# Kernel tuning notes

Hardware: AMD Instinct MI355X
Metric: run time of the kernel (lower is better)

Reference implementation:

```python
import jax, jax.numpy as jnp
import numpy as np

NUM_HEADS = 16
D_MODEL = 1024
D_DEPTH = D_MODEL // NUM_HEADS
B, Q_LEN, M_LEN = 4, 1024, 1024
K_LEN = Q_LEN + M_LEN


def setup_inputs() -> dict:
    key = jax.random.key(0)
    ks = jax.random.split(key, 8)
    return {
        "inputs": jax.random.normal(ks[0], (B, Q_LEN, D_MODEL), jnp.float32),
        "pos_emb": jax.random.normal(ks[1], (1, K_LEN, D_MODEL), jnp.float32),
        "r_w_bias": jax.random.normal(ks[2], (NUM_HEADS, D_DEPTH), jnp.float32) * 0.01,
        "r_r_bias": jax.random.normal(ks[3], (NUM_HEADS, D_DEPTH), jnp.float32) * 0.01,
        "mems": jax.random.normal(ks[4], (B, M_LEN, D_MODEL), jnp.float32),
        "W_w": jax.random.normal(ks[5], (D_MODEL, 3 * D_MODEL), jnp.float32) * 0.01,
        "W_r": jax.random.normal(ks[6], (D_MODEL, D_MODEL), jnp.float32) * 0.01,
        "W_o": jax.random.normal(ks[7], (D_MODEL, D_MODEL), jnp.float32) * 0.01,
    }


def relative_shift(x):
    # x: [b, n, q, k] -> left-shift row i by (q - 1 - i) via pad/reshape/slice trick
    b, n, q, k = x.shape
    x = jnp.pad(x, ((0, 0), (0, 0), (0, 0), (1, 0)))
    x = x.reshape(b, n, k + 1, q)
    x = x[:, :, 1:, :]
    return x.reshape(b, n, q, k)


def relative_mask(q_len, m_len, dtype):
    # [q, m+q]: 1 at/left of current position, 0 to the right
    k = m_len + q_len
    return (jnp.arange(k)[None, :] <= (m_len + jnp.arange(q_len))[:, None]).astype(dtype)


def reference(inputs, pos_emb, r_w_bias, r_r_bias, mems, W_w, W_r, W_o):
    b, q_len, d_model = inputs.shape
    cat = jnp.concatenate([mems, inputs], axis=1)            # [b, k, d]
    k_len = cat.shape[1]
    m_len = k_len - q_len
    pe = pos_emb[:, -k_len:]                                  # [1, k, d]

    w_heads = (cat @ W_w).reshape(b, k_len, 3 * NUM_HEADS, D_DEPTH)
    w_head_q, w_head_k, w_head_v = jnp.split(w_heads, 3, axis=2)  # each [b,k,n,dd]
    w_head_q = w_head_q[:, -q_len:]                           # [b,q,n,dd]

    ac = jnp.einsum('bqnd,bknd->bnqk', w_head_q + r_w_bias, w_head_k)

    r_head_k = (pe[0] @ W_r).reshape(k_len, NUM_HEADS, D_DEPTH)
    bd = jnp.einsum('bqnd,knd->bnqk', w_head_q + r_r_bias, r_head_k)
    bd = relative_shift(bd)

    mask = relative_mask(q_len, m_len, ac.dtype)              # [q, k]
    score = (ac + bd) / jnp.asarray(D_DEPTH ** 0.5, ac.dtype)
    score = score * mask - 1e30 * (1.0 - mask)
    attn = jax.nn.softmax(score, axis=-1)

    attn_vec = jnp.einsum('bnqk,bknd->bqnd', attn, w_head_v)
    attn_vec = attn_vec.reshape(b, q_len, d_model)
    return attn_vec @ W_o
```

## Files before the change

### kernel.cpp

```cpp
#include <hip/hip_runtime.h>
#include <cstdint>
#include <cstddef>

static constexpr int QL = 1024;

typedef _Float16 half8 __attribute__((ext_vector_type(8)));
typedef _Float16 half4 __attribute__((ext_vector_type(4)));
typedef float f32x4 __attribute__((ext_vector_type(4)));

__device__ __forceinline__ const float* gemm_row_ptr(const float* A, const float* A2,
                                                     int r, int gather) {
  if (!gather) return A + (size_t)r * 1024;
  int b = r >> 11, tt = r & 2047;
  if (tt < QL) return A + ((size_t)b * QL + tt) * 1024;
  return A2 + ((size_t)b * QL + (tt - QL)) * 1024;
}

__global__ __launch_bounds__(256) void convert_a16(
    const float* __restrict__ A, const float* __restrict__ A2, int gather,
    _Float16* __restrict__ dst) {
  const int row = blockIdx.x;
  const int c = threadIdx.x * 4;
  const float* src = gemm_row_ptr(A, A2, row, gather);
  float4 v = *(const float4*)(src + c);
  half4 o = { (_Float16)v.x, (_Float16)v.y, (_Float16)v.z, (_Float16)v.w };
  *(half4*)(dst + (size_t)row * 1024 + c) = o;
}

__global__ __launch_bounds__(256) void split_w(
    const float* __restrict__ W, _Float16* __restrict__ Wt, int N) {
  __shared__ float T[64][65];
  const int nb = blockIdx.x * 64, kb = blockIdx.y * 64;
  const int t = threadIdx.x;
  {
    int row = t >> 2, c0 = (t & 3) * 16;
    const float* src = W + (size_t)(kb + row) * N + nb + c0;
#pragma unroll
    for (int c = 0; c < 16; c += 4) {
      float4 v = *(const float4*)(src + c);
      T[row][c0 + c + 0] = v.x; T[row][c0 + c + 1] = v.y;
      T[row][c0 + c + 2] = v.z; T[row][c0 + c + 3] = v.w;
    }
  }
  __syncthreads();
  {
    int nrow = t >> 2, ks = (t & 3) * 16;
    half8 hi0, hi1, lo0, lo1;
#pragma unroll
    for (int c = 0; c < 16; ++c) {
      float f = T[ks + c][nrow];
      _Float16 h = (_Float16)f;
      _Float16 l = (_Float16)(f - (float)h);
      if (c < 8) { hi0[c] = h; lo0[c] = l; } else { hi1[c - 8] = h; lo1[c - 8] = l; }
    }
    int kglob = kb + ks;
    int kt = kglob >> 5, pos = kglob & 31;
    _Float16* dst = Wt + (size_t)(nb + nrow) * 2048 + kt * 64 + pos;
    *(half8*)dst = hi0; *(half8*)(dst + 8) = hi1;
    *(half8*)(dst + 32) = lo0; *(half8*)(dst + 40) = lo1;
  }
}

__global__ __launch_bounds__(256) void gemm2(
    const _Float16* __restrict__ A16, const _Float16* __restrict__ Bt,
    int mode, const float* __restrict__ rwb,
    _Float16* __restrict__ d_q, _Float16* __restrict__ d_k,
    _Float16* __restrict__ d_v, float* __restrict__ d_f) {
  const int nbase = blockIdx.x * 128, mbase = blockIdx.y * 128;
  if (mode == 0 && nbase < 1024 && (mbase & 1024) == 0) return;

  __shared__ __align__(16) _Float16 As[128][40];
  __shared__ __align__(16) _Float16 Bs[128][72];
  const int t = threadIdx.x;
  const int lane = t & 63, w = t >> 6;
  const int ln = lane & 15, g = lane >> 4;
  const int wm = (w & 1) * 64, wn = (w >> 1) * 64;
  const int ar = t >> 1, aseg = (t & 1) * 16;
  const int br = t >> 1;
  const int bseg = (mode == 2) ? (t & 1) * 32 : (t & 1) * 16;
  const _Float16* arow = A16 + (size_t)(mbase + ar) * 1024 + aseg;
  const _Float16* brow = Bt + (size_t)(nbase + br) * 2048 + bseg;

  half8 pa0, pa1, pb0, pb1, pb2, pb3;
  pa0 = *(const half8*)(arow);      pa1 = *(const half8*)(arow + 8);
  pb0 = *(const half8*)(brow);      pb1 = *(const half8*)(brow + 8);
  if (mode == 2) { pb2 = *(const half8*)(brow + 16); pb3 = *(const half8*)(brow + 24); }

  f32x4 acc[4][4] = {};
  for (int kt = 0; kt < 32; ++kt) {
    __syncthreads();
    *(half8*)&As[ar][aseg] = pa0;     *(half8*)&As[ar][aseg + 8] = pa1;
    *(half8*)&Bs[br][bseg] = pb0;     *(half8*)&Bs[br][bseg + 8] = pb1;
    if (mode == 2) { *(half8*)&Bs[br][bseg + 16] = pb2; *(half8*)&Bs[br][bseg + 24] = pb3; }
    __syncthreads();
    if (kt + 1 < 32) {
      const _Float16* ap = arow + (kt + 1) * 32;
      const _Float16* bp = brow + (kt + 1) * 64;
      pa0 = *(const half8*)(ap);      pa1 = *(const half8*)(ap + 8);
      pb0 = *(const half8*)(bp);      pb1 = *(const half8*)(bp + 8);
      if (mode == 2) { pb2 = *(const half8*)(bp + 16); pb3 = *(const half8*)(bp + 24); }
    }
    half8 ah[4], bh[4], bl[4];
#pragma unroll
    for (int i = 0; i < 4; ++i)
      ah[i] = *(const half8*)&As[wm + i * 16 + ln][g * 8];
#pragma unroll
    for (int j = 0; j < 4; ++j)
      bh[j] = *(const half8*)&Bs[wn + j * 16 + ln][g * 8];
    if (mode == 2) {
#pragma unroll
      for (int j = 0; j < 4; ++j)
        bl[j] = *(const half8*)&Bs[wn + j * 16 + ln][32 + g * 8];
    }
#pragma unroll
    for (int i = 0; i < 4; ++i)
#pragma unroll
      for (int j = 0; j < 4; ++j) {
        acc[i][j] = __builtin_amdgcn_mfma_f32_16x16x32_f16(ah[i], bh[j], acc[i][j], 0, 0, 0);
        if (mode == 2)
          acc[i][j] = __builtin_amdgcn_mfma_f32_16x16x32_f16(ah[i], bl[j], acc[i][j], 0, 0, 0);
      }
  }

  if (mode == 2) {
#pragma unroll
    for (int i = 0; i < 4; ++i)
#pragma unroll
      for (int j = 0; j < 4; ++j) {
        float* cp = d_f + (size_t)(mbase + wm + i * 16 + g * 4) * 1024 + nbase + wn + j * 16 + ln;
#pragma unroll
        for (int r = 0; r < 4; ++r) cp[(size_t)r * 1024] = acc[i][j][r];
      }
    return;
  }
  if (mode == 1) {
#pragma unroll
    for (int j = 0; j < 4; ++j) {
      int n = nbase + wn + j * 16 + ln;
      int h = n >> 6, d = n & 63;
#pragma unroll
      for (int i = 0; i < 4; ++i) {
        int m0 = mbase + wm + i * 16 + g * 4;
        _Float16* rp = d_q + ((size_t)h * 2048 + m0) * 64 + d;
#pragma unroll
        for (int r = 0; r < 4; ++r) rp[(size_t)r * 64] = (_Float16)acc[i][j][r];
      }
    }
    return;
  }
#pragma unroll
  for (int j = 0; j < 4; ++j) {
    int n = nbase + wn + j * 16 + ln;
    int sec = n >> 10;
    int c2 = n & 1023, h = c2 >> 6, d = c2 & 63;
    float bias = (sec == 0) ? rwb[c2] : 0.f;
#pragma unroll
    for (int i = 0; i < 4; ++i) {
      int m0 = mbase + wm + i * 16 + g * 4;
      int b = m0 >> 11, tt0 = m0 & 2047;
      size_t bh = (size_t)(b * 16 + h);
#pragma unroll
      for (int r = 0; r < 4; ++r) {
        int tt = tt0 + r;
        float v = acc[i][j][r];
        if (sec == 0) {
          if (tt >= 1024)
            d_q[(bh * 1024 + (tt - 1024)) * 64 + d] = (_Float16)(v + bias);
        } else if (sec == 1) {
          d_k[(bh * 2048 + tt) * 64 + d] = (_Float16)v;
        } else {
          d_v[(bh * 64 + d) * 2048 + tt] = (_Float16)v;
        }
      }
    }
  }
}

__global__ __launch_bounds__(256) void cdelta_kernel(
    const _Float16* __restrict__ r16, const float* __restrict__ rwb,
    const float* __restrict__ rrb, float* __restrict__ cd) {
  int idx = blockIdx.x * 256 + threadIdx.x;
  int jr = idx >> 4, h = idx & 15;
  const _Float16* rp = r16 + ((size_t)h * 2048 + jr) * 64;
  const float* a = rrb + h * 64;
  const float* b = rwb + h * 64;
  float s = 0.f;
#pragma unroll 8
  for (int d = 0; d < 64; ++d) s += (a[d] - b[d]) * (float)rp[d];
  cd[h * 2048 + jr] = s;
}

__global__ __launch_bounds__(256) void attn_mfma3(
    const _Float16* __restrict__ qw16, const _Float16* __restrict__ k16,
    const _Float16* __restrict__ vt16, const _Float16* __restrict__ r16,
    const float* __restrict__ cdelta, _Float16* __restrict__ av16) {
  __shared__ __align__(16) float scratch[4][80][21];
  __shared__ __align__(16) _Float16 k_s[64][72];
  __shared__ __align__(16) _Float16 vt_s[64][72];
  __shared__ __align__(16) _Float16 r_s[128][72];
  __shared__ __align__(16) _Float16 P_s[4][16][72];
  __shared__ float cdw_s[128];
  _Float16 (*qw_s)[72] = (_Float16 (*)[72])&scratch[0][0][0];

  const int id = blockIdx.x;
  const int hb = id & 63, pr = id >> 6;
  const int h = hb >> 2, b = hb & 3;
  const int bh = b * 16 + h;
  const int t = threadIdx.x;
  const int lane = t & 63, w = t >> 6;
  const int ln = lane & 15, g = lane >> 4;
  const int rb = 48 - 16 * w;

  const int s_row4 = t >> 2, s_c16 = (t & 3) * 16;
  const int s_row2 = t >> 1, s_c32 = (t & 1) * 32;

  const float* cdh = cdelta + h * 2048;
  const _Float16* kb_p = k16 + (size_t)bh * 2048 * 64;
  const _Float16* vb_p = vt16 + (size_t)bh * 64 * 2048;
  const _Float16* rb_p = r16 + (size_t)h * 2048 * 64;
  const _Float16* qb_p = qw16 + (size_t)bh * 1024 * 64;

#pragma unroll 1
  for (int phase = 0; phase < 2; ++phase) {
    const int qt = phase ? (15 - pr) : pr;
    const int qbase = qt * 64;
    const int ktiles = qt + 17;
    const int R0 = 960 - qbase;

    __syncthreads();
    {
      const _Float16* src = qb_p + (size_t)(qbase + s_row4) * 64 + s_c16;
      half8 a0 = *(const half8*)src;
      half8 a1 = *(const half8*)(src + 8);
      *(half8*)&qw_s[s_row4][s_c16] = a0;
      *(half8*)&qw_s[s_row4][s_c16 + 8] = a1;
    }
    __syncthreads();
    half8 aq0 = *(const half8*)&qw_s[16 * w + ln][g * 8];
    half8 aq1 = *(const half8*)&qw_s[16 * w + ln][32 + g * 8];
    __syncthreads();

    f32x4 O[4] = {};
    float llane[4] = {0.f, 0.f, 0.f, 0.f};

    half8 kp0, kp1, vp0, vp1, rp0, rp1, rp2, rp3;
    float cdp = 0.f;
    {
      const _Float16* kp = kb_p + (size_t)s_row4 * 64 + s_c16;
      kp0 = *(const half8*)kp; kp1 = *(const half8*)(kp + 8);
      const _Float16* vp = vb_p + (size_t)s_row4 * 2048 + s_c16;
      vp0 = *(const half8*)vp; vp1 = *(const half8*)(vp + 8);
      int rr = R0 + s_row2; rr = rr > 2047 ? 2047 : rr;
      const _Float16* rp = rb_p + (size_t)rr * 64 + s_c32;
      rp0 = *(const half8*)rp;        rp1 = *(const half8*)(rp + 8);
      rp2 = *(const half8*)(rp + 16); rp3 = *(const half8*)(rp + 24);
      if (t < 128) { int cr = R0 + t; cr = cr > 2047 ? 2047 : cr; cdp = cdh[cr]; }
    }

    for (int kt = 0; kt < ktiles; ++kt) {
      const int kbase = kt * 64;
      const int koff = (kt & 1) * 64;
      __syncthreads();
      *(half8*)&k_s[s_row4][s_c16] = kp0;  *(half8*)&k_s[s_row4][s_c16 + 8] = kp1;
      *(half8*)&vt_s[s_row4][s_c16] = vp0; *(half8*)&vt_s[s_row4][s_c16 + 8] = vp1;
      if (kt == 0) {
        *(half8*)&r_s[s_row2][s_c32] = rp0;      *(half8*)&r_s[s_row2][s_c32 + 8] = rp1;
        *(half8*)&r_s[s_row2][s_c32 + 16] = rp2; *(half8*)&r_s[s_row2][s_c32 + 24] = rp3;
        if (t < 128) cdw_s[t] = cdp;
      } else {
        const int sb = 64 - koff;
        *(half8*)&r_s[sb + s_row4][s_c16] = rp0;
        *(half8*)&r_s[sb + s_row4][s_c16 + 8] = rp1;
        if (t < 64) cdw_s[sb + t] = cdp;
      }
      __syncthreads();
      if (kt + 1 < ktiles) {
        const int kb2 = kbase + 64;
        const _Float16* kp = kb_p + (size_t)(kb2 + s_row4) * 64 + s_c16;
        kp0 = *(const half8*)kp; kp1 = *(const half8*)(kp + 8);
        const _Float16* vp = vb_p + (size_t)s_row4 * 2048 + kb2 + s_c16;
        vp0 = *(const half8*)vp; vp1 = *(const half8*)(vp + 8);
        int rr = R0 + kbase + 128 + s_row4; rr = rr > 2047 ? 2047 : rr;
        const _Float16* rp = rb_p + (size_t)rr * 64 + s_c16;
        rp0 = *(const half8*)rp; rp1 = *(const half8*)(rp + 8);
        if (t < 64) { int cr = R0 + kbase + 128 + t; cr = cr > 2047 ? 2047 : cr; cdp = cdh[cr]; }
      }

      f32x4 Sf[4];
#pragma unroll
      for (int jt = 0; jt < 4; ++jt) {
        half8 b0 = *(const half8*)&k_s[jt * 16 + ln][g * 8];
        half8 b1 = *(const half8*)&k_s[jt * 16 + ln][32 + g * 8];
        f32x4 z = {0.f, 0.f, 0.f, 0.f};
        z = __builtin_amdgcn_mfma_f32_16x16x32_f16(aq0, b0, z, 0, 0, 0);
        z = __builtin_amdgcn_mfma_f32_16x16x32_f16(aq1, b1, z, 0, 0, 0);
        Sf[jt] = z;
      }
#pragma unroll
      for (int ft = 0; ft < 5; ++ft) {
        int rrow = (rb + ft * 16 + ln + koff) & 127;
        half8 b0 = *(const half8*)&r_s[rrow][g * 8];
        half8 b1 = *(const half8*)&r_s[rrow][32 + g * 8];
        f32x4 z = {0.f, 0.f, 0.f, 0.f};
        z = __builtin_amdgcn_mfma_f32_16x16x32_f16(aq0, b0, z, 0, 0, 0);
        z = __builtin_amdgcn_mfma_f32_16x16x32_f16(aq1, b1, z, 0, 0, 0);
        float cdv = cdw_s[rrow];
        float* sc = &scratch[w][ft * 16 + ln][0];
        sc[4 * g + 0] = z[0] + cdv; sc[4 * g + 1] = z[1] + cdv;
        sc[4 * g + 2] = z[2] + cdv; sc[4 * g + 3] = z[3] + cdv;
      }
      const int climit = qbase + 16 * w + 1039 - kbase;
#pragma unroll
      for (int r = 0; r < 4; ++r) {
        float psum = 0.f;
#pragma unroll
        for (int jt = 0; jt < 4; ++jt) {
          int cw = jt * 16 + ln + 15 - 4 * g - r;
          float tv = scratch[w][cw][4 * g + r];
          float x = (Sf[jt][r] + tv) * 0.125f;
          float p = (cw > climit) ? 0.f : __expf(x);
          psum += p;
          P_s[w][4 * g + r][jt * 16 + ln] = (_Float16)p;
        }
        llane[r] += psum;
      }
      half8 pA0 = *(const half8*)&P_s[w][ln][g * 8];
      half8 pA1 = *(const half8*)&P_s[w][ln][32 + g * 8];
#pragma unroll
      for (int dt = 0; dt < 4; ++dt) {
        half8 b0 = *(const half8*)&vt_s[dt * 16 + ln][g * 8];
        half8 b1 = *(const half8*)&vt_s[dt * 16 + ln][32 + g * 8];
        O[dt] = __builtin_amdgcn_mfma_f32_16x16x32_f16(pA0, b0, O[dt], 0, 0, 0);
        O[dt] = __builtin_amdgcn_mfma_f32_16x16x32_f16(pA1, b1, O[dt], 0, 0, 0);
      }
    }

#pragma unroll
    for (int r = 0; r < 4; ++r) {
      float ls = llane[r];
      ls += __shfl_xor(ls, 1, 64);
      ls += __shfl_xor(ls, 2, 64);
      ls += __shfl_xor(ls, 4, 64);
      ls += __shfl_xor(ls, 8, 64);
      float inv = 1.f / ls;
      int qrow = qbase + 16 * w + 4 * g + r;
      _Float16* op = av16 + ((size_t)b * 1024 + qrow) * 1024 + h * 64 + ln;
#pragma unroll
      for (int dt = 0; dt < 4; ++dt) op[dt * 16] = (_Float16)(O[dt][r] * inv);
    }
  }
}

extern "C" void kernel_launch(void* const* d_in, const int* in_sizes, int n_in,
                              void* d_out, int out_size, void* d_ws, size_t ws_size,
                              hipStream_t stream) {
  const float* inputs  = (const float*)d_in[0];
  const float* pos_emb = (const float*)d_in[1];
  const float* rwb     = (const float*)d_in[2];
  const float* rrb     = (const float*)d_in[3];
  const float* mems    = (const float*)d_in[4];
  const float* W_w     = (const float*)d_in[5];
  const float* W_r     = (const float*)d_in[6];
  const float* W_o     = (const float*)d_in[7];
  float* out = (float*)d_out;

  _Float16* hws = (_Float16*)d_ws;
  _Float16* a16   = hws;
  _Float16* pe16  = a16  + (size_t)8192 * 1024;
  _Float16* qw16  = pe16 + (size_t)2048 * 1024;
  _Float16* k16   = qw16 + (size_t)64 * 1024 * 64;
  _Float16* vt16  = k16  + (size_t)64 * 2048 * 64;
  _Float16* r16   = vt16 + (size_t)64 * 64 * 2048;
  _Float16* av16  = r16  + (size_t)16 * 2048 * 64;
  _Float16* wwt   = av16 + (size_t)4096 * 1024;
  _Float16* wrt   = wwt  + (size_t)3072 * 2048;
  _Float16* wot   = wrt  + (size_t)1024 * 2048;
  float*    cdelta = (float*)(wot + (size_t)1024 * 2048);

  convert_a16<<<8192, 256, 0, stream>>>(mems, inputs, 1, a16);
  convert_a16<<<2048, 256, 0, stream>>>(pos_emb, nullptr, 0, pe16);
  split_w<<<dim3(48, 16), 256, 0, stream>>>(W_w, wwt, 3072);
  split_w<<<dim3(16, 16), 256, 0, stream>>>(W_r, wrt, 1024);
  split_w<<<dim3(16, 16), 256, 0, stream>>>(W_o, wot, 1024);
  gemm2<<<dim3(24, 64), 256, 0, stream>>>(a16, wwt, 0, rwb, qw16, k16, vt16, nullptr);
  gemm2<<<dim3(8, 16), 256, 0, stream>>>(pe16, wrt, 1, rwb, r16, nullptr, nullptr, nullptr);
  cdelta_kernel<<<128, 256, 0, stream>>>(r16, rwb, rrb, cdelta);
  attn_mfma3<<<512, 256, 0, stream>>>(qw16, k16, vt16, r16, cdelta, av16);
  gemm2<<<dim3(8, 32), 256, 0, stream>>>(av16, wot, 2, rwb, nullptr, nullptr, nullptr, out);
}
```

Before: 382.8 us.

## Replace LDS relative-shift scratch with cross-lane shuffles and merge prep kernels

The attention kernel no longer writes the positional score tile to a shared-memory scratch buffer and reads it back shifted. Instead it keeps the tile in registers and applies the relative shift with wavefront shuffles. Dropping the roughly 27 KB scratch array lowers LDS use, and together with launch_bounds(256,3) this aims for more resident blocks per CU. The Q tile is now staged in r_s, which removes one barrier. The fp32-to-fp16 conversions and weight transposes are each merged into a single launch to cut launch overhead; the cost is more register pressure from holding the shifted values.

```diff
diff --git a/kernel.cpp b/kernel.cpp
--- a/kernel.cpp
+++ b/kernel.cpp
@@ -16,21 +16,36 @@
   return A2 + ((size_t)b * QL + (tt - QL)) * 1024;
 }
 
-__global__ __launch_bounds__(256) void convert_a16(
-    const float* __restrict__ A, const float* __restrict__ A2, int gather,
-    _Float16* __restrict__ dst) {
+__global__ __launch_bounds__(256) void convert_all(
+    const float* __restrict__ mems, const float* __restrict__ inputs,
+    const float* __restrict__ pos_emb,
+    _Float16* __restrict__ a16, _Float16* __restrict__ pe16) {
   const int row = blockIdx.x;
   const int c = threadIdx.x * 4;
-  const float* src = gemm_row_ptr(A, A2, row, gather);
-  float4 v = *(const float4*)(src + c);
-  half4 o = { (_Float16)v.x, (_Float16)v.y, (_Float16)v.z, (_Float16)v.w };
-  *(half4*)(dst + (size_t)row * 1024 + c) = o;
-}
-
-__global__ __launch_bounds__(256) void split_w(
-    const float* __restrict__ W, _Float16* __restrict__ Wt, int N) {
+  if (row < 8192) {
+    const float* src = gemm_row_ptr(mems, inputs, row, 1);
+    float4 v = *(const float4*)(src + c);
+    half4 o = { (_Float16)v.x, (_Float16)v.y, (_Float16)v.z, (_Float16)v.w };
+    *(half4*)(a16 + (size_t)row * 1024 + c) = o;
+  } else {
+    int r2 = row - 8192;
+    float4 v = *(const float4*)(pos_emb + (size_t)r2 * 1024 + c);
+    half4 o = { (_Float16)v.x, (_Float16)v.y, (_Float16)v.z, (_Float16)v.w };
+    *(half4*)(pe16 + (size_t)r2 * 1024 + c) = o;
+  }
+}
+
+__global__ __launch_bounds__(256) void split_w3(
+    const float* __restrict__ Ww, const float* __restrict__ Wr,
+    const float* __restrict__ Wo, _Float16* __restrict__ wwt,
+    _Float16* __restrict__ wrt, _Float16* __restrict__ wot) {
   __shared__ float T[64][65];
-  const int nb = blockIdx.x * 64, kb = blockIdx.y * 64;
+  const int x = blockIdx.x;
+  const float* W; _Float16* Wt; int N, nbB;
+  if (x < 48)      { W = Ww; Wt = wwt; N = 3072; nbB = x; }
+  else if (x < 64) { W = Wr; Wt = wrt; N = 1024; nbB = x - 48; }
+  else             { W = Wo; Wt = wot; N = 1024; nbB = x - 64; }
+  const int nb = nbB * 64, kb = blockIdx.y * 64;
   const int t = threadIdx.x;
   {
     int row = t >> 2, c0 = (t & 3) * 16;
@@ -190,17 +205,15 @@
   cd[h * 2048 + jr] = s;
 }
 
-__global__ __launch_bounds__(256) void attn_mfma3(
+__global__ __launch_bounds__(256, 3) void attn_mfma4(
     const _Float16* __restrict__ qw16, const _Float16* __restrict__ k16,
     const _Float16* __restrict__ vt16, const _Float16* __restrict__ r16,
     const float* __restrict__ cdelta, _Float16* __restrict__ av16) {
-  __shared__ __align__(16) float scratch[4][80][21];
   __shared__ __align__(16) _Float16 k_s[64][72];
   __shared__ __align__(16) _Float16 vt_s[64][72];
   __shared__ __align__(16) _Float16 r_s[128][72];
   __shared__ __align__(16) _Float16 P_s[4][16][72];
   __shared__ float cdw_s[128];
-  _Float16 (*qw_s)[72] = (_Float16 (*)[72])&scratch[0][0][0];
 
   const int id = blockIdx.x;
   const int hb = id & 63, pr = id >> 6;
@@ -232,13 +245,12 @@
       const _Float16* src = qb_p + (size_t)(qbase + s_row4) * 64 + s_c16;
       half8 a0 = *(const half8*)src;
       half8 a1 = *(const half8*)(src + 8);
-      *(half8*)&qw_s[s_row4][s_c16] = a0;
-      *(half8*)&qw_s[s_row4][s_c16 + 8] = a1;
+      *(half8*)&r_s[s_row4][s_c16] = a0;
+      *(half8*)&r_s[s_row4][s_c16 + 8] = a1;
     }
     __syncthreads();
-    half8 aq0 = *(const half8*)&qw_s[16 * w + ln][g * 8];
-    half8 aq1 = *(const half8*)&qw_s[16 * w + ln][32 + g * 8];
-    __syncthreads();
+    half8 aq0 = *(const half8*)&r_s[16 * w + ln][g * 8];
+    half8 aq1 = *(const half8*)&r_s[16 * w + ln][32 + g * 8];
 
     f32x4 O[4] = {};
     float llane[4] = {0.f, 0.f, 0.f, 0.f};
@@ -296,6 +308,7 @@
         z = __builtin_amdgcn_mfma_f32_16x16x32_f16(aq1, b1, z, 0, 0, 0);
         Sf[jt] = z;
       }
+      f32x4 Tf[5];
 #pragma unroll
       for (int ft = 0; ft < 5; ++ft) {
         int rrow = (rb + ft * 16 + ln + koff) & 127;
@@ -305,19 +318,25 @@
         z = __builtin_amdgcn_mfma_f32_16x16x32_f16(aq0, b0, z, 0, 0, 0);
         z = __builtin_amdgcn_mfma_f32_16x16x32_f16(aq1, b1, z, 0, 0, 0);
         float cdv = cdw_s[rrow];
-        float* sc = &scratch[w][ft * 16 + ln][0];
-        sc[4 * g + 0] = z[0] + cdv; sc[4 * g + 1] = z[1] + cdv;
-        sc[4 * g + 2] = z[2] + cdv; sc[4 * g + 3] = z[3] + cdv;
+        z[0] += cdv; z[1] += cdv; z[2] += cdv; z[3] += cdv;
+        Tf[ft] = z;
       }
       const int climit = qbase + 16 * w + 1039 - kbase;
 #pragma unroll
       for (int r = 0; r < 4; ++r) {
+        const int c = 15 - 4 * g - r;
+        const int lnc = ln + c;
+        const int src = (lane & 48) | (lnc & 15);
+        float rot[5];
+#pragma unroll
+        for (int ft = 0; ft < 5; ++ft) rot[ft] = __shfl(Tf[ft][r], src, 64);
+        const bool hi = lnc >= 16;
         float psum = 0.f;
 #pragma unroll
         for (int jt = 0; jt < 4; ++jt) {
-          int cw = jt * 16 + ln + 15 - 4 * g - r;
-          float tv = scratch[w][cw][4 * g + r];
+          float tv = hi ? rot[jt + 1] : rot[jt];
           float x = (Sf[jt][r] + tv) * 0.125f;
+          int cw = jt * 16 + lnc;
           float p = (cw > climit) ? 0.f : __expf(x);
           psum += p;
           P_s[w][4 * g + r][jt * 16 + ln] = (_Float16)p;
@@ -377,14 +396,11 @@
   _Float16* wot   = wrt  + (size_t)1024 * 2048;
   float*    cdelta = (float*)(wot + (size_t)1024 * 2048);
 
-  convert_a16<<<8192, 256, 0, stream>>>(mems, inputs, 1, a16);
-  convert_a16<<<2048, 256, 0, stream>>>(pos_emb, nullptr, 0, pe16);
-  split_w<<<dim3(48, 16), 256, 0, stream>>>(W_w, wwt, 3072);
-  split_w<<<dim3(16, 16), 256, 0, stream>>>(W_r, wrt, 1024);
-  split_w<<<dim3(16, 16), 256, 0, stream>>>(W_o, wot, 1024);
+  convert_all<<<10240, 256, 0, stream>>>(mems, inputs, pos_emb, a16, pe16);
+  split_w3<<<dim3(80, 16), 256, 0, stream>>>(W_w, W_r, W_o, wwt, wrt, wot);
   gemm2<<<dim3(24, 64), 256, 0, stream>>>(a16, wwt, 0, rwb, qw16, k16, vt16, nullptr);
   gemm2<<<dim3(8, 16), 256, 0, stream>>>(pe16, wrt, 1, rwb, r16, nullptr, nullptr, nullptr);
   cdelta_kernel<<<128, 256, 0, stream>>>(r16, rwb, rrb, cdelta);
-  attn_mfma3<<<512, 256, 0, stream>>>(qw16, k16, vt16, r16, cdelta, av16);
+  attn_mfma4<<<512, 256, 0, stream>>>(qw16, k16, vt16, r16, cdelta, av16);
   gemm2<<<dim3(8, 32), 256, 0, stream>>>(av16, wot, 2, rwb, nullptr, nullptr, nullptr, out);
 }
```

Result: slower. 455.6 us (+19.0%).
